# Kernel optimization log

Hardware: AMD Instinct MI355X
Metric: run time of the kernel (lower is better)

The kernel has to match this reference:

```python
import jax, jax.numpy as jnp
import numpy as np
from jax import lax

LEA, STE, GRA = 8, 8, 8
C_DIM = LEA + STE + GRA          # 24
AUX_DIM = 5
IN_DIM = C_DIM + AUX_DIM         # 29


def setup_inputs() -> dict:
    key = jax.random.key(0)
    ks = jax.random.split(key, 12)
    B, T = 1024, 366
    X = jax.random.uniform(ks[0], (B, T, 4), dtype=jnp.float32)
    ORY = jax.random.uniform(ks[1], (B, T, 7), dtype=jnp.float32)
    W_redis = jax.random.normal(ks[2], (C_DIM * C_DIM, IN_DIM), dtype=jnp.float32)
    b_redis = jax.random.normal(ks[3], (C_DIM * C_DIM,), dtype=jnp.float32)
    W_part = jax.random.normal(ks[4], (C_DIM, IN_DIM), dtype=jnp.float32)
    b_part = jax.random.normal(ks[5], (C_DIM,), dtype=jnp.float32)
    W_cons = jax.random.normal(ks[6], (C_DIM, IN_DIM), dtype=jnp.float32)
    b_cons = jax.random.normal(ks[7], (C_DIM,), dtype=jnp.float32)
    W_assim = jax.random.normal(ks[8], (1, IN_DIM), dtype=jnp.float32)
    b_assim = jax.random.normal(ks[9], (1,), dtype=jnp.float32)
    c2a_par = jnp.ones((C_DIM,), dtype=jnp.float32)
    g2y_par = jnp.ones((GRA,), dtype=jnp.float32)
    return dict(X=X, ORY=ORY, W_redis=W_redis, b_redis=b_redis,
                W_part=W_part, b_part=b_part, W_cons=W_cons, b_cons=b_cons,
                W_assim=W_assim, b_assim=b_assim, c2a_par=c2a_par, g2y_par=g2y_par)


def _redis_prior():
    # ones over C_cell part, zeros over aux except index -4 (rad) = 1
    p = jnp.concatenate([jnp.ones(C_DIM, jnp.float32), jnp.zeros(AUX_DIM, jnp.float32)])
    return p.at[IN_DIM - 4].set(1.0)


def _forward(X, ORY, W_redis, b_redis, W_part, b_part, W_cons, b_cons,
             W_assim, b_assim, c2a_par, g2y_par):
    B, T, _ = X.shape
    # ---- preprocessing ----
    N_cum = jnp.cumsum(X[:, :, 3], axis=-1)[..., None]          # [B,T,1]
    t_ave = jnp.mean(X[:, :, 1:3], axis=-1, keepdims=True)       # [B,T,1]
    dvs = ORY[:, :, :1]
    rad = X[:, :, 0:1]
    tmax = X[:, :, 1:2]
    tmin = X[:, :, 2:3]
    FRPAR = 0.5
    eff = 0.54 - (jnp.clip(t_ave * 50.0, 10.0, 40.0) - 10.0) / 30.0 * (0.54 - 0.36)
    R2C_par = (40000.0 / 20000.0) * FRPAR * eff / 3.6 * (12.0 / 44.0)
    C_potential = rad * R2C_par                                  # [B,T,1]
    AUX = jnp.concatenate([dvs, rad, tmax, tmin, N_cum], axis=-1)  # [B,T,5]

    redis_prior = _redis_prior()
    # all other input priors are ones, all output priors are zeros -> no-ops

    def redis_gate(x):
        z = (x * redis_prior) @ W_redis.T + b_redis
        return jax.nn.softmax(z.reshape(-1, C_DIM, C_DIM), axis=-1)

    def step(C_cell, ts):
        aux_t, cpot_t = ts                                       # [B,5], [B,1]
        x = jnp.concatenate([C_cell, aux_t], axis=1)             # [B,29]
        assim = jax.nn.sigmoid(x @ W_assim.T + b_assim)          # [B,1]
        part = jax.nn.softmax(x @ W_part.T + b_part, axis=-1)    # [B,24]
        cons = jax.nn.sigmoid(x @ W_cons.T + b_cons)             # [B,24]
        redis = redis_gate(x)                                    # [B,24,24]
        C_in = assim * cpot_t                                    # [B,1]
        C_cell = C_cell + C_in * part
        C_cell = C_cell * (1.0 - cons)
        C_cell = jnp.einsum('bi,bij->bj', C_cell, redis)
        x2 = jnp.concatenate([C_cell, aux_t], axis=1)
        redis2 = redis_gate(x2)
        C_conv = jnp.einsum('bi,bij->bj', C_cell, redis2)
        return C_cell, (C_cell, C_conv)

    aux_seq = jnp.transpose(AUX[:, :T - 1, :], (1, 0, 2))        # [T-1,B,5]
    cpot_seq = jnp.transpose(C_potential[:, :T - 1, :], (1, 0, 2))
    C0 = jnp.zeros((B, C_DIM), X.dtype)
    _, (C_all, C_conv_all) = lax.scan(step, C0, (aux_seq, cpot_seq))
    C_cell_all = jnp.transpose(C_all, (1, 0, 2))                 # [B,T-1,24]
    C_cell_convergence_all = jnp.transpose(C_conv_all, (1, 0, 2))

    pai = jnp.sum(jnp.abs(C_cell_all * c2a_par), axis=2, keepdims=True)
    lea = jnp.sum(C_cell_all[:, :, 0:LEA], axis=2, keepdims=True) / 0.419
    ste = jnp.sum(C_cell_all[:, :, LEA:LEA + STE], axis=2, keepdims=True) / 0.431
    gra = jnp.sum(C_cell_all[:, :, LEA + STE:C_DIM], axis=2, keepdims=True) / 0.487
    agb = lea + ste + gra
    yie = jnp.sum(jnp.abs(C_cell_all[:, :, LEA + STE:C_DIM] * g2y_par),
                  axis=2, keepdims=True) / 0.487
    all_day = jnp.concatenate([dvs[:, 1:], pai, lea, ste, gra, agb, yie], axis=2)
    all_day = jnp.concatenate([ORY[:, :1, :], all_day], axis=1)  # [B,T,7]
    return all_day, C_cell_all, C_cell_convergence_all


def reference(X, ORY, W_redis, b_redis, W_part, b_part, W_cons, b_cons,
              W_assim, b_assim, c2a_par, g2y_par):
    return _forward(X, ORY, W_redis, b_redis, W_part, b_part, W_cons, b_cons,
                    W_assim, b_assim, c2a_par, g2y_par)
```

## Files before the change

### kernel.cpp

```cpp
#include <hip/hip_runtime.h>

#define B_ 1024
#define T_ 366
#define NS_ 365
#define CD_ 24

__device__ __forceinline__ float sigm(float x) { return __fdividef(1.f, 1.f + __expf(-x)); }
__device__ __forceinline__ float rl(float v, int k) {
    return __int_as_float(__builtin_amdgcn_readlane(__float_as_int(v), k));
}

__global__ void mclstm_pack(const float* __restrict__ Wr, const float* __restrict__ br,
                            const float* __restrict__ Wp, const float* __restrict__ bp,
                            const float* __restrict__ Wc, const float* __restrict__ bc,
                            const float* __restrict__ Wa, const float* __restrict__ ba,
                            float* __restrict__ Wpk, float* __restrict__ Apk) {
    const int e = blockIdx.x * 64 + threadIdx.x;
    if (e < 576) {
#pragma unroll
        for (int k = 0; k < 24; ++k) Wpk[e * 32 + k] = Wr[e * 29 + k];
        Wpk[e * 32 + 24] = Wr[e * 29 + 25];
        Wpk[e * 32 + 25] = br[e];
#pragma unroll
        for (int k = 26; k < 32; ++k) Wpk[e * 32 + k] = 0.f;
    } else if (e < 625) {
        const int r = e - 576;
#pragma unroll
        for (int k = 0; k < 29; ++k)
            Apk[r * 32 + k] = (r < 24) ? Wp[r * 29 + k] : (r < 48) ? Wc[(r - 24) * 29 + k] : Wa[k];
        Apk[r * 32 + 29] = (r < 24) ? bp[r] : (r < 48) ? bc[r - 24] : ba[0];
        Apk[r * 32 + 30] = 0.f; Apk[r * 32 + 31] = 0.f;
    }
}

__global__ __attribute__((amdgpu_flat_work_group_size(128, 128), amdgpu_waves_per_eu(2, 2)))
void mclstm_main(const float* __restrict__ X, const float* __restrict__ ORY,
                 const float* __restrict__ Wpk, const float* __restrict__ Apk,
                 const float* __restrict__ c2a, const float* __restrict__ g2y,
                 float* __restrict__ allday, float* __restrict__ Ccell,
                 float* __restrict__ Cconv)
{
    __shared__ __align__(16) float zb1[672], zb2[672];
    __shared__ __align__(16) float pb1[672], pb2[672];
    __shared__ __align__(16) float cbuf[24];
    __shared__ float cmb[24];

    const int tid = threadIdx.x;
    const int l = tid & 63, wv = tid >> 6;
    const int b = blockIdx.x;

    float wrg[4][24], wrad[4], brg[4];
    int za[4];
#pragma unroll
    for (int j = 0; j < 4; ++j) {
        const int e = tid + 128 * j;
        const float4* wp = (const float4*)(Wpk + (size_t)e * 32);
#pragma unroll
        for (int q = 0; q < 6; ++q) {
            const float4 v = wp[q];
            wrg[j][4*q] = v.x; wrg[j][4*q+1] = v.y; wrg[j][4*q+2] = v.z; wrg[j][4*q+3] = v.w;
        }
        const float4 t = wp[6];
        wrad[j] = t.x; brg[j] = t.y;
        za[j] = (e / 24) * 28 + (e % 24);
    }
    float ext[32];
    {
        const float4* p = (const float4*)((wv == 0) ? (Wpk + (size_t)(512 + l) * 32)
                                                    : (Apk + (size_t)((l < 49) ? l : 48) * 32));
#pragma unroll
        for (int q = 0; q < 8; ++q) {
            const float4 v = p[q];
            ext[4*q] = v.x; ext[4*q+1] = v.y; ext[4*q+2] = v.z; ext[4*q+3] = v.w;
        }
    }
    const int za4 = ((512 + l) / 24) * 28 + (512 + l) % 24;

    const int rc = l >> 1, hh = l & 1;
    const bool evn = ((l & 1) == 0) && (l < 48);
    const float c2 = evn ? c2a[l >> 1] : 0.f;
    const float gy = (evn && l >= 32) ? g2y[(l >> 1) - 16] : 0.f;

    const float* xrow = X + (size_t)b * T_ * 4;
    const float* orow = ORY + (size_t)b * T_ * 7;

    if (tid < 7) allday[(size_t)b * T_ * 7 + tid] = orow[tid];
    if (tid < 24) cbuf[tid] = 0.f;
    __syncthreads();

    float Ncum = 0.f, rp = 0.f;
    float4 xc = *(const float4*)xrow;
    float dvsc = orow[0];

    for (int u = 0; u <= NS_; ++u) {
        const bool do1 = (u < NS_), doCv = (u > 0);

        const int un = (u + 1 <= NS_) ? (u + 1) : NS_;
        const float4 xn = *(const float4*)(xrow + un * 4);
        const float dn = orow[un * 7];

        const float ra = xc.x;

        float Cs[24];
#pragma unroll
        for (int q = 0; q < 6; ++q) {
            const float4 v = ((const float4*)cbuf)[q];
            Cs[4*q] = v.x; Cs[4*q+1] = v.y; Cs[4*q+2] = v.z; Cs[4*q+3] = v.w;
        }
        const float mlt1 = cbuf[rc];

#pragma unroll
        for (int j = 0; j < 4; ++j) {
            float p0 = brg[j], p1 = 0.f, p2 = 0.f, p3 = 0.f;
#pragma unroll
            for (int k = 0; k < 24; k += 4) {
                p0 = fmaf(wrg[j][k],   Cs[k],   p0);
                p1 = fmaf(wrg[j][k+1], Cs[k+1], p1);
                p2 = fmaf(wrg[j][k+2], Cs[k+2], p2);
                p3 = fmaf(wrg[j][k+3], Cs[k+3], p3);
            }
            const float D = (p0 + p1) + (p2 + p3);
            if (do1)  zb1[za[j]] = fmaf(wrad[j], ra, D);
            if (doCv) zb2[za[j]] = fmaf(wrad[j], rp, D);
        }

        if (wv == 0) {
            float p0 = ext[25], p1 = 0.f, p2 = 0.f, p3 = 0.f;
#pragma unroll
            for (int k = 0; k < 24; k += 4) {
                p0 = fmaf(ext[k],   Cs[k],   p0);
                p1 = fmaf(ext[k+1], Cs[k+1], p1);
                p2 = fmaf(ext[k+2], Cs[k+2], p2);
                p3 = fmaf(ext[k+3], Cs[k+3], p3);
            }
            const float D = (p0 + p1) + (p2 + p3);
            if (do1)  zb1[za4] = fmaf(ext[24], ra, D);
            if (doCv) zb2[za4] = fmaf(ext[24], rp, D);
        } else if (do1) {
            Ncum += xc.w;
            const float tave = 0.5f * (xc.y + xc.z);
            const float clm = fminf(fmaxf(tave * 50.f, 10.f), 40.f);
            const float eff = 0.54f - (clm - 10.f) * (0.18f / 30.f);
            const float cpot = ra * (eff * (2.f * 0.5f / 3.6f * (12.f / 44.f)));

            float z = ext[29];
#pragma unroll
            for (int k = 0; k < 24; ++k) z = fmaf(ext[k], Cs[k], z);
            z = fmaf(ext[24], dvsc, z);
            z = fmaf(ext[25], ra, z);
            z = fmaf(ext[26], xc.y, z);
            z = fmaf(ext[27], xc.z, z);
            z = fmaf(ext[28], Ncum, z);

            float pm = (l < 24) ? z : -1e30f;
#pragma unroll
            for (int o = 1; o < 32; o <<= 1) pm = fmaxf(pm, __shfl_xor(pm, o, 32));
            float pe = (l < 24) ? __expf(z - pm) : 0.f;
            float ps = pe;
#pragma unroll
            for (int o = 1; o < 32; o <<= 1) ps += __shfl_xor(ps, o, 32);
            const float conz = __shfl(z, 24 + (l & 31), 64);
            const float asmz = __shfl(z, 48, 64);
            if (l < 24) {
                const float part = __fdividef(pe, ps);
                cmb[l] = (cbuf[l] + sigm(asmz) * cpot * part) * (1.f - sigm(conz));
            }
        }
        __syncthreads();

        float ssum = 0.f;
        {
            const bool act = (l < 48) && (wv ? doCv : do1);
            if (act) {
                const float* zs = wv ? zb2 : zb1;
                float* pbk = wv ? pb2 : pb1;
                const float4* z4 = (const float4*)(zs + rc * 28 + hh * 12);
                float z[12];
#pragma unroll
                for (int q = 0; q < 3; ++q) {
                    const float4 v = z4[q];
                    z[4*q] = v.x; z[4*q+1] = v.y; z[4*q+2] = v.z; z[4*q+3] = v.w;
                }
                float m = z[0];
#pragma unroll
                for (int i = 1; i < 12; ++i) m = fmaxf(m, z[i]);
                m = fmaxf(m, __shfl_xor(m, 1));
                float ss = 0.f;
#pragma unroll
                for (int i = 0; i < 12; ++i) { z[i] = __expf(z[i] - m); ss += z[i]; }
                ss += __shfl_xor(ss, 1);
                const float mult = wv ? mlt1 : cmb[rc];
                const float f = __fdividef(mult, ss);
#pragma unroll
                for (int i = 0; i < 12; ++i) pbk[(hh * 12 + i) * 28 + rc] = z[i] * f;

                const float4* p4 = (const float4*)(pbk + rc * 28 + hh * 12);
#pragma unroll
                for (int i = 0; i < 3; ++i) {
                    const float4 v = p4[i];
                    ssum += (v.x + v.y) + (v.z + v.w);
                }
                ssum += __shfl_xor(ssum, 1);
                if (hh == 0) {
                    if (wv) {
                        Cconv[((size_t)b * NS_ + (u - 1)) * CD_ + rc] = ssum;
                    } else {
                        cbuf[rc] = ssum;
                        Ccell[((size_t)b * NS_ + u) * CD_ + rc] = ssum;
                    }
                }
            }
        }
        if (wv == 0 && do1) {
            const float cv = evn ? ssum : 0.f;
            const float pv = fabsf(cv * c2);
            const float yv = fabsf(cv * gy);
            float a16 = cv, p16 = pv, y16 = yv;
#pragma unroll
            for (int o = 1; o < 16; o <<= 1) {
                a16 += __shfl_xor(a16, o, 16);
                p16 += __shfl_xor(p16, o, 16);
                y16 += __shfl_xor(y16, o, 16);
            }
            const float pai = rl(p16, 0) + rl(p16, 16) + rl(p16, 32);
            const float lea = rl(a16, 0)  * (1.f / 0.419f);
            const float ste = rl(a16, 16) * (1.f / 0.431f);
            const float gra = rl(a16, 32) * (1.f / 0.487f);
            const float yie = rl(y16, 32) * (1.f / 0.487f);
            const float agb = lea + ste + gra;
            if (l < 7) {
                float val = dn;
                val = (l == 1) ? pai : val;
                val = (l == 2) ? lea : val;
                val = (l == 3) ? ste : val;
                val = (l == 4) ? gra : val;
                val = (l == 5) ? agb : val;
                val = (l == 6) ? yie : val;
                allday[((size_t)b * T_ + (u + 1)) * 7 + l] = val;
            }
        }
        __syncthreads();
        rp = ra; xc = xn; dvsc = dn;
    }
}

extern "C" void kernel_launch(void* const* d_in, const int* in_sizes, int n_in,
                              void* d_out, int out_size, void* d_ws, size_t ws_size,
                              hipStream_t stream) {
    const float* X   = (const float*)d_in[0];
    const float* ORY = (const float*)d_in[1];
    const float* Wr  = (const float*)d_in[2];
    const float* br  = (const float*)d_in[3];
    const float* Wp  = (const float*)d_in[4];
    const float* bp  = (const float*)d_in[5];
    const float* Wc  = (const float*)d_in[6];
    const float* bc  = (const float*)d_in[7];
    const float* Wa  = (const float*)d_in[8];
    const float* ba  = (const float*)d_in[9];
    const float* c2a = (const float*)d_in[10];
    const float* g2y = (const float*)d_in[11];

    float* allday = (float*)d_out;
    float* Ccell  = allday + (size_t)B_ * T_ * 7;
    float* Cconv  = Ccell + (size_t)B_ * NS_ * CD_;

    float* Wpk = (float*)d_ws;
    float* Apk = Wpk + 576 * 32;

    hipLaunchKernelGGL(mclstm_pack, dim3(10), dim3(64), 0, stream,
                       Wr, br, Wp, bp, Wc, bc, Wa, ba, Wpk, Apk);
    hipLaunchKernelGGL(mclstm_main, dim3(B_), dim3(128), 0, stream,
                       X, ORY, Wpk, Apk, c2a, g2y, allday, Ccell, Cconv);
}
```

Baseline: 731.3 us.

## Move per-step output reductions to a separate kernel and fold log2e into weights

The per-timestep pai/lea/ste/gra/agb/yie shuffle reductions and allday writes leave the serial recurrence loop. A new fully parallel kernel rebuilds them afterwards from the stored Ccell. All packed weights and biases are also prescaled by log2(e) so the softmax and sigmoid use exp2f directly, dropping a multiply per exponential. The cost is a third kernel launch and an extra read of the whole Ccell tensor from memory.

```diff
diff --git a/kernel.cpp b/kernel.cpp
--- a/kernel.cpp
+++ b/kernel.cpp
@@ -4,8 +4,11 @@
 #define T_ 366
 #define NS_ 365
 #define CD_ 24
-
-__device__ __forceinline__ float sigm(float x) { return __fdividef(1.f, 1.f + __expf(-x)); }
+#define NTASK (B_ * NS_)
+
+__device__ __forceinline__ float sigm2(float x) {
+    return __fdividef(1.f, 1.f + exp2f(-x));
+}
 __device__ __forceinline__ float rl(float v, int k) {
     return __int_as_float(__builtin_amdgcn_readlane(__float_as_int(v), k));
 }
@@ -15,20 +18,21 @@
                             const float* __restrict__ Wc, const float* __restrict__ bc,
                             const float* __restrict__ Wa, const float* __restrict__ ba,
                             float* __restrict__ Wpk, float* __restrict__ Apk) {
+    const float S = 1.44269504088896341f;
     const int e = blockIdx.x * 64 + threadIdx.x;
     if (e < 576) {
 #pragma unroll
-        for (int k = 0; k < 24; ++k) Wpk[e * 32 + k] = Wr[e * 29 + k];
-        Wpk[e * 32 + 24] = Wr[e * 29 + 25];
-        Wpk[e * 32 + 25] = br[e];
+        for (int k = 0; k < 24; ++k) Wpk[e * 32 + k] = Wr[e * 29 + k] * S;
+        Wpk[e * 32 + 24] = Wr[e * 29 + 25] * S;
+        Wpk[e * 32 + 25] = br[e] * S;
 #pragma unroll
         for (int k = 26; k < 32; ++k) Wpk[e * 32 + k] = 0.f;
     } else if (e < 625) {
         const int r = e - 576;
 #pragma unroll
         for (int k = 0; k < 29; ++k)
-            Apk[r * 32 + k] = (r < 24) ? Wp[r * 29 + k] : (r < 48) ? Wc[(r - 24) * 29 + k] : Wa[k];
-        Apk[r * 32 + 29] = (r < 24) ? bp[r] : (r < 48) ? bc[r - 24] : ba[0];
+            Apk[r * 32 + k] = ((r < 24) ? Wp[r * 29 + k] : (r < 48) ? Wc[(r - 24) * 29 + k] : Wa[k]) * S;
+        Apk[r * 32 + 29] = ((r < 24) ? bp[r] : (r < 48) ? bc[r - 24] : ba[0]) * S;
         Apk[r * 32 + 30] = 0.f; Apk[r * 32 + 31] = 0.f;
     }
 }
@@ -36,9 +40,7 @@
 __global__ __attribute__((amdgpu_flat_work_group_size(128, 128), amdgpu_waves_per_eu(2, 2)))
 void mclstm_main(const float* __restrict__ X, const float* __restrict__ ORY,
                  const float* __restrict__ Wpk, const float* __restrict__ Apk,
-                 const float* __restrict__ c2a, const float* __restrict__ g2y,
-                 float* __restrict__ allday, float* __restrict__ Ccell,
-                 float* __restrict__ Cconv)
+                 float* __restrict__ Ccell, float* __restrict__ Cconv)
 {
     __shared__ __align__(16) float zb1[672], zb2[672];
     __shared__ __align__(16) float pb1[672], pb2[672];
@@ -77,14 +79,10 @@
     const int za4 = ((512 + l) / 24) * 28 + (512 + l) % 24;
 
     const int rc = l >> 1, hh = l & 1;
-    const bool evn = ((l & 1) == 0) && (l < 48);
-    const float c2 = evn ? c2a[l >> 1] : 0.f;
-    const float gy = (evn && l >= 32) ? g2y[(l >> 1) - 16] : 0.f;
 
     const float* xrow = X + (size_t)b * T_ * 4;
     const float* orow = ORY + (size_t)b * T_ * 7;
 
-    if (tid < 7) allday[(size_t)b * T_ * 7 + tid] = orow[tid];
     if (tid < 24) cbuf[tid] = 0.f;
     __syncthreads();
 
@@ -155,7 +153,7 @@
             float pm = (l < 24) ? z : -1e30f;
 #pragma unroll
             for (int o = 1; o < 32; o <<= 1) pm = fmaxf(pm, __shfl_xor(pm, o, 32));
-            float pe = (l < 24) ? __expf(z - pm) : 0.f;
+            float pe = (l < 24) ? exp2f(z - pm) : 0.f;
             float ps = pe;
 #pragma unroll
             for (int o = 1; o < 32; o <<= 1) ps += __shfl_xor(ps, o, 32);
@@ -163,12 +161,11 @@
             const float asmz = __shfl(z, 48, 64);
             if (l < 24) {
                 const float part = __fdividef(pe, ps);
-                cmb[l] = (cbuf[l] + sigm(asmz) * cpot * part) * (1.f - sigm(conz));
+                cmb[l] = (cbuf[l] + sigm2(asmz) * cpot * part) * (1.f - sigm2(conz));
             }
         }
         __syncthreads();
 
-        float ssum = 0.f;
         {
             const bool act = (l < 48) && (wv ? doCv : do1);
             if (act) {
@@ -187,13 +184,14 @@
                 m = fmaxf(m, __shfl_xor(m, 1));
                 float ss = 0.f;
 #pragma unroll
-                for (int i = 0; i < 12; ++i) { z[i] = __expf(z[i] - m); ss += z[i]; }
+                for (int i = 0; i < 12; ++i) { z[i] = exp2f(z[i] - m); ss += z[i]; }
                 ss += __shfl_xor(ss, 1);
                 const float mult = wv ? mlt1 : cmb[rc];
                 const float f = __fdividef(mult, ss);
 #pragma unroll
                 for (int i = 0; i < 12; ++i) pbk[(hh * 12 + i) * 28 + rc] = z[i] * f;
 
+                float ssum = 0.f;
                 const float4* p4 = (const float4*)(pbk + rc * 28 + hh * 12);
 #pragma unroll
                 for (int i = 0; i < 3; ++i) {
@@ -211,37 +209,48 @@
                 }
             }
         }
-        if (wv == 0 && do1) {
-            const float cv = evn ? ssum : 0.f;
-            const float pv = fabsf(cv * c2);
-            const float yv = fabsf(cv * gy);
-            float a16 = cv, p16 = pv, y16 = yv;
-#pragma unroll
-            for (int o = 1; o < 16; o <<= 1) {
-                a16 += __shfl_xor(a16, o, 16);
-                p16 += __shfl_xor(p16, o, 16);
-                y16 += __shfl_xor(y16, o, 16);
-            }
-            const float pai = rl(p16, 0) + rl(p16, 16) + rl(p16, 32);
-            const float lea = rl(a16, 0)  * (1.f / 0.419f);
-            const float ste = rl(a16, 16) * (1.f / 0.431f);
-            const float gra = rl(a16, 32) * (1.f / 0.487f);
-            const float yie = rl(y16, 32) * (1.f / 0.487f);
-            const float agb = lea + ste + gra;
-            if (l < 7) {
-                float val = dn;
-                val = (l == 1) ? pai : val;
-                val = (l == 2) ? lea : val;
-                val = (l == 3) ? ste : val;
-                val = (l == 4) ? gra : val;
-                val = (l == 5) ? agb : val;
-                val = (l == 6) ? yie : val;
-                allday[((size_t)b * T_ + (u + 1)) * 7 + l] = val;
-            }
-        }
         __syncthreads();
         rp = ra; xc = xn; dvsc = dn;
     }
+}
+
+__global__ __launch_bounds__(256) void mclstm_allday(
+    const float* __restrict__ ORY, const float* __restrict__ c2a,
+    const float* __restrict__ g2y, const float* __restrict__ Ccell,
+    float* __restrict__ allday) {
+    const int tid = blockIdx.x * 256 + threadIdx.x;
+    if (tid < B_) {
+#pragma unroll
+        for (int k = 0; k < 7; ++k)
+            allday[(size_t)tid * T_ * 7 + k] = ORY[(size_t)tid * T_ * 7 + k];
+    }
+    if (tid >= NTASK) return;
+    const int b = tid / NS_;
+    const int t = tid - b * NS_;
+
+    const float* Cp = Ccell + (size_t)tid * CD_;
+    float C[24];
+#pragma unroll
+    for (int q = 0; q < 6; ++q) {
+        const float4 v = *(const float4*)(Cp + 4 * q);
+        C[4 * q] = v.x; C[4 * q + 1] = v.y; C[4 * q + 2] = v.z; C[4 * q + 3] = v.w;
+    }
+    float pai = 0.f;
+#pragma unroll
+    for (int c = 0; c < 24; ++c) pai += fabsf(C[c] * c2a[c]);
+    float lea = 0.f, ste = 0.f, gra = 0.f, yie = 0.f;
+#pragma unroll
+    for (int c = 0; c < 8; ++c) lea += C[c];
+#pragma unroll
+    for (int c = 8; c < 16; ++c) ste += C[c];
+#pragma unroll
+    for (int c = 16; c < 24; ++c) { gra += C[c]; yie += fabsf(C[c] * g2y[c - 16]); }
+    lea /= 0.419f; ste /= 0.431f; gra /= 0.487f; yie /= 0.487f;
+    const float agb = lea + ste + gra;
+
+    float* ad = allday + ((size_t)b * T_ + (t + 1)) * 7;
+    ad[0] = ORY[((size_t)b * T_ + (t + 1)) * 7];
+    ad[1] = pai; ad[2] = lea; ad[3] = ste; ad[4] = gra; ad[5] = agb; ad[6] = yie;
 }
 
 extern "C" void kernel_launch(void* const* d_in, const int* in_sizes, int n_in,
@@ -270,5 +279,7 @@
     hipLaunchKernelGGL(mclstm_pack, dim3(10), dim3(64), 0, stream,
                        Wr, br, Wp, bp, Wc, bc, Wa, ba, Wpk, Apk);
     hipLaunchKernelGGL(mclstm_main, dim3(B_), dim3(128), 0, stream,
-                       X, ORY, Wpk, Apk, c2a, g2y, allday, Ccell, Cconv);
-}
+                       X, ORY, Wpk, Apk, Ccell, Cconv);
+    hipLaunchKernelGGL(mclstm_allday, dim3(NTASK / 256), dim3(256), 0, stream,
+                       ORY, c2a, g2y, Ccell, allday);
+}
```

Measured after the change: 678.6 us. -7.2%, faster.
